# Kernel tuning notes

Measured on AMD Instinct MI355X. Metric: run time of the kernel, lower is better.

## Reference

```python
import jax, jax.numpy as jnp
import numpy as np

jax.config.update("jax_enable_x64", True)

# Module constants (from MySDELayer.call / run_model)
NUM_TRAJ = 512
DT = 2.0 ** (-8)          # deltat
NSTEPS = 255              # len(arange(0,1,DT)) - 1
OMEGA = 5.0265            # params[0]
GAMMA = 0.36              # params[2]
SQG = float(np.sqrt(GAMMA))


def setup_inputs() -> dict:
    key = jax.random.key(0)
    k1, k2 = jax.random.split(key)
    inputs = jax.random.normal(k1, (32, 1), dtype=jnp.float32)
    # unit-normal Wiener increments; scaled by sqrt(DT) inside reference
    wvec = jax.random.normal(k2, (32 * NUM_TRAJ, NSTEPS, 2), dtype=jnp.float32)
    return {"inputs": inputs, "wvec": wvec}


def _sde_probs(eps, dw):
    """Euler-Maruyama integration of the Genois qubit heterodyne SDE in Bloch
    coordinates (d=3 state, m=2 Wiener channels, complex128 as in the original),
    followed by unwrap to rho and Pauli-expectation probabilities.
    eps: [N] complex128 (per-trajectory middle parameter, e.g. detuning)
    dw:  [N, NSTEPS, 2] complex128 Wiener increments (stddev sqrt(DT))
    returns probs [N, NSTEPS+1, 6] float64
    """
    N = eps.shape[0]
    x0 = jnp.broadcast_to(jnp.array([0.0, 0.0, 1.0], dtype=jnp.complex128), (N, 3))

    def step(x, dwt):  # x: [N,3], dwt: [N,2]
        xx, yy, zz = x[:, 0], x[:, 1], x[:, 2]
        # drift: Rabi drive OMEGA about x, detuning eps about z, dephasing GAMMA
        drift = jnp.stack([
            -eps * yy - GAMMA * xx,
            eps * xx - OMEGA * zz - GAMMA * yy,
            OMEGA * yy,
        ], axis=1)
        # heterodyne measurement backaction (two quadratures)
        b1 = SQG * jnp.stack([-xx * zz, -yy * zz, 1.0 - zz * zz], axis=1)
        b2 = SQG * jnp.stack([-yy, xx, jnp.zeros_like(xx)], axis=1)
        xn = x + drift * DT + b1 * dwt[:, 0:1] + b2 * dwt[:, 1:2]
        return xn, xn

    _, xs = jax.lax.scan(step, x0, jnp.swapaxes(dw, 0, 1))  # [NSTEPS, N, 3]
    xvec = jnp.concatenate([x0[None], xs], axis=0)           # [T, N, 3]
    xvec = jnp.transpose(xvec, (1, 0, 2))                    # [N, T, 3]

    # unwrap_x_to_rho: rho = 0.5*(I + r.sigma) as length-4 vec
    rho = jnp.stack([
        0.5 * (1.0 + xvec[..., 2]),
        0.5 * (xvec[..., 0] - 1j * xvec[..., 1]),
        0.5 * (xvec[..., 0] + 1j * xvec[..., 1]),
        0.5 * (1.0 - xvec[..., 2]),
    ], axis=-1)                                              # [N, T, 4]

    # calc_exp with Pauli matrices
    ex = jnp.real(rho[..., 1] + rho[..., 2])
    ey = jnp.real(1j * (rho[..., 1] - rho[..., 2]))
    ez = jnp.real(rho[..., 0] - rho[..., 3])
    px, py, pz = 0.5 * (ex + 1.0), 0.5 * (ey + 1.0), 0.5 * (ez + 1.0)
    return jnp.stack([px, 1.0 - px, py, 1.0 - py, pz, 1.0 - pz], axis=2)  # [N,T,6]


def reference(inputs, wvec):
    B = inputs.shape[0]
    # tf.tile(inputs, [num_traj, 1])[:, 0] -> trajectory-major replication
    eps = jnp.tile(inputs, (NUM_TRAJ, 1))[:, 0].astype(jnp.complex128)  # [N]
    dw = (wvec * np.sqrt(DT)).astype(jnp.complex128)                    # [N,255,2]
    probs = _sde_probs(eps, dw)                                         # [N,T,6]
    probs_by_params = probs.reshape(B, NUM_TRAJ, probs.shape[1], 6)
    return jnp.mean(probs_by_params, axis=1)                            # [B,T,6]
```

## Files before the change

kernel.cpp:

```cpp
#include <hip/hip_runtime.h>

#define NSTEPS 255
#define TPTS   256
#define NTRAJ  16384
#define NBLK   256
#define CH     15

#define GAMMA_F 0.36f
#define OMEGA_F 5.0265f
#define DT_F    0.00390625f
#define CW      0.0375f
#define GD      (GAMMA_F * DT_F)
#define OD      (OMEGA_F * DT_F)

typedef __fp16 half2v __attribute__((ext_vector_type(2)));
typedef float  f32x2  __attribute__((ext_vector_type(2)));

__device__ __forceinline__ unsigned pk2(float a, float b) {
  half2v h = __builtin_amdgcn_cvt_pkrtz(a, b);
  return __builtin_bit_cast(unsigned, h);
}

template<int CTRL, int RM>
__device__ __forceinline__ float dpp_add(float v) {
  int sh = __builtin_amdgcn_update_dpp(0, __float_as_int(v), CTRL, RM, 0xf, true);
  return v + __int_as_float(sh);
}

__device__ __forceinline__ float wave_sum64(float v) {
  v = dpp_add<0x111, 0xf>(v);
  v = dpp_add<0x112, 0xf>(v);
  v = dpp_add<0x114, 0xf>(v);
  v = dpp_add<0x118, 0xf>(v);
  v = dpp_add<0x142, 0xa>(v);
  v = dpp_add<0x143, 0xc>(v);
  return v;
}

#define STEP(w2, tidx) {                                                        \
  const float w0  = (w2).x * CW;                                                \
  const f32x2 w1n = nCW2 * (w2).y;                        \
  const f32x2 sw  = __builtin_shufflevector(v, v, 1, 0);             \
  f32x2 t = __builtin_elementwise_fma(epack, sw, v);                            \
  t = __builtin_elementwise_fma(mGD2, v, t);                                    \
  const f32x2 p   = v * z;                                                      \
  const f32x2 mw0 = {-w0, -w0};                                                 \
  t = __builtin_elementwise_fma(p, mw0, t);                                     \
  t = __builtin_elementwise_fma(sw, w1n, t);                                    \
  t[1] = __builtin_fmaf(-OD, z, t[1]);                                          \
  const float a = __builtin_fmaf(OD, v[1], z);                                  \
  const float r = __builtin_fmaf(-(z * z), w0, w0);                             \
  v = t; z = a + r;                                                             \
  sp[(size_t)((tidx) - 1) * NTRAJ] = make_uint2(pk2(v[0], v[1]), pk2(z, 0.0f)); \
}

#define LOADC(BUF, CHUNK_) {                                                    \
  _Pragma("unroll")                                                             \
  for (int i_ = 0; i_ < CH; ++i_) BUF[i_] = wrow[(CHUNK_) * CH + i_];           \
}

#define PROC(BUF) {                                                             \
  _Pragma("unroll")                                                             \
  for (int i_ = 0; i_ < CH; ++i_) STEP(BUF[i_], tb + i_)                        \
  tb += CH;                                                                     \
}

__global__ __launch_bounds__(64) void sde_integrate(const float* __restrict__ inp,
                                                    const float* __restrict__ wvec,
                                                    uint2* __restrict__ buf) {
  const int g    = blockIdx.x;
  const int lane = threadIdx.x;
  const float eps = inp[lane & 31];
  const f32x2 epack = {-eps * DT_F, eps * DT_F};
  const f32x2 mGD2  = {-GD, -GD};
  const f32x2 nCW2  = {-CW, CW};

  const float2* __restrict__ wrow =
      reinterpret_cast<const float2*>(wvec) + (size_t)(g * 64 + lane) * NSTEPS;
  uint2* __restrict__ sp = buf + (size_t)(g * 64 + lane);

  f32x2 v = {0.0f, 0.0f};
  float z = 1.0f;

  float2 bufA[CH], bufB[CH], bufC[CH];

  LOADC(bufA, 0);
  LOADC(bufB, 1);
  int tb = 1;
  #pragma unroll 1
  for (int k = 0; k < 5; ++k) {
    LOADC(bufC, 3 * k + 2); PROC(bufA);
    LOADC(bufA, 3 * k + 3); PROC(bufB);
    LOADC(bufB, 3 * k + 4); PROC(bufC);
  }
  PROC(bufA);
  PROC(bufB);
}

__global__ __launch_bounds__(256) void sde_reduce(const uint2* __restrict__ buf,
                                                  float* __restrict__ out) {
  const int wid  = (blockIdx.x << 2) | (threadIdx.x >> 6);
  const int lane = threadIdx.x & 63;
  const int b = wid >> 8;
  const int t = wid & 255;
  float* o = out + (size_t)wid * 6;

  if (t == 0) {
    if (lane < 6) o[lane] = (lane == 4) ? 1.0f : ((lane == 5) ? 0.0f : 0.5f);
    return;
  }

  const uint2* base = buf + (size_t)(t - 1) * NTRAJ + (b << 9) + lane;
  float sx = 0.0f, sy = 0.0f, sz = 0.0f;
  #pragma unroll
  for (int k = 0; k < 8; ++k) {
    const uint2 w = base[(size_t)k * 64];
    const half2v xy = __builtin_bit_cast(half2v, w.x);
    const half2v zp = __builtin_bit_cast(half2v, w.y);
    sx += (float)xy[0];
    sy += (float)xy[1];
    sz += (float)zp[0];
  }
  sx = wave_sum64(sx);
  sy = wave_sum64(sy);
  sz = wave_sum64(sz);

  if (lane == 63) {
    const float inv = 1.0f / 512.0f;
    const float mx = sx * inv, my = sy * inv, mz = sz * inv;
    o[0] = 0.5f * (1.0f + mx);
    o[1] = 0.5f * (1.0f - mx);
    o[2] = 0.5f * (1.0f + my);
    o[3] = 0.5f * (1.0f - my);
    o[4] = 0.5f * (1.0f + mz);
    o[5] = 0.5f * (1.0f - mz);
  }
}

extern "C" void kernel_launch(void* const* d_in, const int* in_sizes, int n_in,
                              void* d_out, int out_size, void* d_ws, size_t ws_size,
                              hipStream_t stream) {
  (void)in_sizes; (void)n_in; (void)out_size; (void)ws_size;
  const float* inp  = (const float*)d_in[0];
  const float* wvec = (const float*)d_in[1];
  float* out  = (float*)d_out;
  uint2* buf  = (uint2*)d_ws;

  sde_integrate<<<NBLK, 64, 0, stream>>>(inp, wvec, buf);
  sde_reduce<<<2048, 256, 0, stream>>>(buf, out);
}
```

Measured before the change: 27.81 us.

## Stage Wiener increments through double-buffered LDS with coalesced global loads

Each trajectory used to read its own strided 2040-byte row of Wiener increments directly, so a wave's loads were uncoalesced. Now 16 lanes cooperatively load contiguous 8-byte pieces of each row into a padded, double-buffered LDS tile. Each thread then reads its own row back from LDS as float4 pairs, with the next chunk's global loads issued during the current chunk's compute. This adds LDS traffic and a per-chunk __syncthreads, and the fixed chunk offsets and bounds must cover exactly 255 steps.

```diff
diff --git a/kernel.cpp b/kernel.cpp
--- a/kernel.cpp
+++ b/kernel.cpp
@@ -4,7 +4,7 @@
 #define TPTS   256
 #define NTRAJ  16384
 #define NBLK   256
-#define CH     15
+#define ROWB   2040
 
 #define GAMMA_F 0.36f
 #define OMEGA_F 5.0265f
@@ -12,6 +12,9 @@
 #define CW      0.0375f
 #define GD      (GAMMA_F * DT_F)
 #define OD      (OMEGA_F * DT_F)
+
+#define LROW  144
+#define LBUF  (64 * LROW)
 
 typedef __fp16 half2v __attribute__((ext_vector_type(2)));
 typedef float  f32x2  __attribute__((ext_vector_type(2)));
@@ -37,9 +40,9 @@
   return v;
 }
 
-#define STEP(w2, tidx) {                                                        \
-  const float w0  = (w2).x * CW;                                                \
-  const f32x2 w1n = nCW2 * (w2).y;                        \
+#define STEP2(wx_, wy_) {                                                       \
+  const float w0  = (wx_) * CW;                                                 \
+  const f32x2 w1n = nCW2 * (wy_);                         \
   const f32x2 sw  = __builtin_shufflevector(v, v, 1, 0);             \
   f32x2 t = __builtin_elementwise_fma(epack, sw, v);                            \
   t = __builtin_elementwise_fma(mGD2, v, t);                                    \
@@ -48,53 +51,68 @@
   t = __builtin_elementwise_fma(p, mw0, t);                                     \
   t = __builtin_elementwise_fma(sw, w1n, t);                                    \
   t[1] = __builtin_fmaf(-OD, z, t[1]);                                          \
-  const float a = __builtin_fmaf(OD, v[1], z);                                  \
-  const float r = __builtin_fmaf(-(z * z), w0, w0);                             \
-  v = t; z = a + r;                                                             \
-  sp[(size_t)((tidx) - 1) * NTRAJ] = make_uint2(pk2(v[0], v[1]), pk2(z, 0.0f)); \
+  const float a_ = __builtin_fmaf(OD, v[1], z);                                 \
+  const float r_ = __builtin_fmaf(-(z * z), w0, w0);                            \
+  v = t; z = a_ + r_;                                                           \
+  *sp = make_uint2(pk2(v[0], v[1]), pk2(z, 0.0f));                              \
+  sp += NTRAJ;                                                                  \
 }
 
-#define LOADC(BUF, CHUNK_) {                                                    \
+#define GLOAD(co) {                                                             \
   _Pragma("unroll")                                                             \
-  for (int i_ = 0; i_ < CH; ++i_) BUF[i_] = wrow[(CHUNK_) * CH + i_];           \
+  for (int i_ = 0; i_ < 16; ++i_)                                               \
+    r2[i_] = *(const float2*)(wbp + (size_t)i_ * (4 * ROWB) + (co));            \
 }
 
-#define PROC(BUF) {                                                             \
+#define LDSWRITE() {                                                            \
   _Pragma("unroll")                                                             \
-  for (int i_ = 0; i_ < CH; ++i_) STEP(BUF[i_], tb + i_)                        \
-  tb += CH;                                                                     \
+  for (int i_ = 0; i_ < 16; ++i_)                                               \
+    *(float2*)(smem + wl + i_ * (4 * LROW)) = r2[i_];                           \
+}
+
+#define CHUNK(NK) {                                                             \
+  _Pragma("unroll")                                                             \
+  for (int p_ = 0; p_ < 8; ++p_) {                                              \
+    const float4 wv = *(const float4*)(smem + rl + p_ * 16);                    \
+    STEP2(wv.x, wv.y);                                                          \
+    if (2 * p_ + 1 < (NK)) STEP2(wv.z, wv.w);                                   \
+  }                                                                             \
 }
 
 __global__ __launch_bounds__(64) void sde_integrate(const float* __restrict__ inp,
                                                     const float* __restrict__ wvec,
                                                     uint2* __restrict__ buf) {
-  const int g    = blockIdx.x;
-  const int lane = threadIdx.x;
-  const float eps = inp[lane & 31];
+  __shared__ alignas(16) char smem[2 * LBUF];
+  const int g = blockIdx.x, l = threadIdx.x;
+  const float eps = inp[l & 31];
   const f32x2 epack = {-eps * DT_F, eps * DT_F};
   const f32x2 mGD2  = {-GD, -GD};
   const f32x2 nCW2  = {-CW, CW};
 
-  const float2* __restrict__ wrow =
-      reinterpret_cast<const float2*>(wvec) + (size_t)(g * 64 + lane) * NSTEPS;
-  uint2* __restrict__ sp = buf + (size_t)(g * 64 + lane);
+  const char* wbp = (const char*)wvec
+      + (size_t)(g * 64 + (l >> 4)) * ROWB + (l & 15) * 8;
+  unsigned wl = (unsigned)((l >> 4) * LROW + (l & 15) * 8);
+  unsigned rl = (unsigned)(l * LROW);
+  uint2* __restrict__ sp = buf + (g * 64 + l);
 
   f32x2 v = {0.0f, 0.0f};
   float z = 1.0f;
+  float2 r2[16];
 
-  float2 bufA[CH], bufB[CH], bufC[CH];
+  GLOAD(0);
+  LDSWRITE();
+  __syncthreads();
+  GLOAD(120);
+  CHUNK(15);
 
-  LOADC(bufA, 0);
-  LOADC(bufB, 1);
-  int tb = 1;
   #pragma unroll 1
-  for (int k = 0; k < 5; ++k) {
-    LOADC(bufC, 3 * k + 2); PROC(bufA);
-    LOADC(bufA, 3 * k + 3); PROC(bufB);
-    LOADC(bufB, 3 * k + 4); PROC(bufC);
+  for (int c = 1; c <= 15; ++c) {
+    wl ^= LBUF; rl ^= LBUF;
+    LDSWRITE();
+    __syncthreads();
+    if (c < 15) GLOAD(128 * c + 120);
+    CHUNK(16);
   }
-  PROC(bufA);
-  PROC(bufB);
 }
 
 __global__ __launch_bounds__(256) void sde_reduce(const uint2* __restrict__ buf,
```

Result: slower. 30.23 us (+8.7%).

## Stage trajectory states in LDS and pre-reduce per block before finalize

Applied to the files above, without the earlier changes.

Instead of writing every trajectory's packed state for every timestep to global workspace and reducing it in a second kernel, each 64-lane block now stores its states in shared memory and sums the 64 trajectories per timestep inside the block. The much smaller per-block partial sums are then combined across the 8 blocks of each batch by a small finalize kernel. This removes roughly 33MB of global write and read traffic. In exchange it uses about 132KB of LDS per block, which limits occupancy, and it adds a serial 64-element per-thread reduction tail after the integration loop.

```diff
diff --git a/kernel.cpp b/kernel.cpp
--- a/kernel.cpp
+++ b/kernel.cpp
@@ -13,6 +13,8 @@
 #define GD      (GAMMA_F * DT_F)
 #define OD      (OMEGA_F * DT_F)
 
+#define PITCH  520
+
 typedef __fp16 half2v __attribute__((ext_vector_type(2)));
 typedef float  f32x2  __attribute__((ext_vector_type(2)));
 
@@ -21,23 +23,7 @@
   return __builtin_bit_cast(unsigned, h);
 }
 
-template<int CTRL, int RM>
-__device__ __forceinline__ float dpp_add(float v) {
-  int sh = __builtin_amdgcn_update_dpp(0, __float_as_int(v), CTRL, RM, 0xf, true);
-  return v + __int_as_float(sh);
-}
-
-__device__ __forceinline__ float wave_sum64(float v) {
-  v = dpp_add<0x111, 0xf>(v);
-  v = dpp_add<0x112, 0xf>(v);
-  v = dpp_add<0x114, 0xf>(v);
-  v = dpp_add<0x118, 0xf>(v);
-  v = dpp_add<0x142, 0xa>(v);
-  v = dpp_add<0x143, 0xc>(v);
-  return v;
-}
-
-#define STEP(w2, tidx) {                                                        \
+#define STEP2(w2, ii_) {                                                        \
   const float w0  = (w2).x * CW;                                                \
   const f32x2 w1n = nCW2 * (w2).y;                        \
   const f32x2 sw  = __builtin_shufflevector(v, v, 1, 0);             \
@@ -48,10 +34,10 @@
   t = __builtin_elementwise_fma(p, mw0, t);                                     \
   t = __builtin_elementwise_fma(sw, w1n, t);                                    \
   t[1] = __builtin_fmaf(-OD, z, t[1]);                                          \
-  const float a = __builtin_fmaf(OD, v[1], z);                                  \
-  const float r = __builtin_fmaf(-(z * z), w0, w0);                             \
-  v = t; z = a + r;                                                             \
-  sp[(size_t)((tidx) - 1) * NTRAJ] = make_uint2(pk2(v[0], v[1]), pk2(z, 0.0f)); \
+  const float a_ = __builtin_fmaf(OD, v[1], z);                                 \
+  const float r_ = __builtin_fmaf(-(z * z), w0, w0);                            \
+  v = t; z = a_ + r_;                                                           \
+  *(uint2*)(sb + (ii_) * PITCH) = make_uint2(pk2(v[0], v[1]), pk2(z, 0.0f));    \
 }
 
 #define LOADC(BUF, CHUNK_) {                                                    \
@@ -61,23 +47,23 @@
 
 #define PROC(BUF) {                                                             \
   _Pragma("unroll")                                                             \
-  for (int i_ = 0; i_ < CH; ++i_) STEP(BUF[i_], tb + i_)                        \
-  tb += CH;                                                                     \
+  for (int i_ = 0; i_ < CH; ++i_) STEP2(BUF[i_], i_)                            \
+  sb += CH * PITCH;                                                             \
 }
 
 __global__ __launch_bounds__(64) void sde_integrate(const float* __restrict__ inp,
                                                     const float* __restrict__ wvec,
-                                                    uint2* __restrict__ buf) {
-  const int g    = blockIdx.x;
-  const int lane = threadIdx.x;
-  const float eps = inp[lane & 31];
+                                                    float* __restrict__ partial) {
+  __shared__ alignas(16) char smem[NSTEPS * PITCH];
+  const int g = blockIdx.x, l = threadIdx.x;
+  const float eps = inp[l & 31];
   const f32x2 epack = {-eps * DT_F, eps * DT_F};
   const f32x2 mGD2  = {-GD, -GD};
   const f32x2 nCW2  = {-CW, CW};
 
   const float2* __restrict__ wrow =
-      reinterpret_cast<const float2*>(wvec) + (size_t)(g * 64 + lane) * NSTEPS;
-  uint2* __restrict__ sp = buf + (size_t)(g * 64 + lane);
+      reinterpret_cast<const float2*>(wvec) + (size_t)(g * 64 + l) * NSTEPS;
+  char* sb = smem + l * 8;
 
   f32x2 v = {0.0f, 0.0f};
   float z = 1.0f;
@@ -86,7 +72,6 @@
 
   LOADC(bufA, 0);
   LOADC(bufB, 1);
-  int tb = 1;
   #pragma unroll 1
   for (int k = 0; k < 5; ++k) {
     LOADC(bufC, 3 * k + 2); PROC(bufA);
@@ -95,46 +80,57 @@
   }
   PROC(bufA);
   PROC(bufB);
+
+  __syncthreads();
+
+  #pragma unroll
+  for (int k = 0; k < 4; ++k) {
+    const int s = l + 64 * k;
+    if (s < NSTEPS) {
+      const char* rb = smem + (size_t)s * PITCH;
+      float fx = 0.0f, fy = 0.0f, fz = 0.0f;
+      #pragma unroll
+      for (int j = 0; j < 64; ++j) {
+        const uint2 u = *(const uint2*)(rb + j * 8);
+        const half2v xy = __builtin_bit_cast(half2v, u.x);
+        const half2v zp = __builtin_bit_cast(half2v, u.y);
+        fx += (float)xy[0];
+        fy += (float)xy[1];
+        fz += (float)zp[0];
+      }
+      float* p = partial + ((size_t)g * NSTEPS + s) * 3;
+      p[0] = fx; p[1] = fy; p[2] = fz;
+    }
+  }
 }
 
-__global__ __launch_bounds__(256) void sde_reduce(const uint2* __restrict__ buf,
-                                                  float* __restrict__ out) {
-  const int wid  = (blockIdx.x << 2) | (threadIdx.x >> 6);
-  const int lane = threadIdx.x & 63;
-  const int b = wid >> 8;
-  const int t = wid & 255;
-  float* o = out + (size_t)wid * 6;
+__global__ __launch_bounds__(256) void sde_finalize(const float* __restrict__ partial,
+                                                    float* __restrict__ out) {
+  const int idx = blockIdx.x * blockDim.x + threadIdx.x;
+  const int b = idx >> 8;
+  const int t = idx & 255;
+  float* o = out + (size_t)idx * 6;
 
   if (t == 0) {
-    if (lane < 6) o[lane] = (lane == 4) ? 1.0f : ((lane == 5) ? 0.0f : 0.5f);
+    o[0] = 0.5f; o[1] = 0.5f; o[2] = 0.5f; o[3] = 0.5f;
+    o[4] = 1.0f; o[5] = 0.0f;
     return;
   }
 
-  const uint2* base = buf + (size_t)(t - 1) * NTRAJ + (b << 9) + lane;
   float sx = 0.0f, sy = 0.0f, sz = 0.0f;
   #pragma unroll
-  for (int k = 0; k < 8; ++k) {
-    const uint2 w = base[(size_t)k * 64];
-    const half2v xy = __builtin_bit_cast(half2v, w.x);
-    const half2v zp = __builtin_bit_cast(half2v, w.y);
-    sx += (float)xy[0];
-    sy += (float)xy[1];
-    sz += (float)zp[0];
+  for (int j = 0; j < 8; ++j) {
+    const float* p = partial + ((size_t)(b * 8 + j) * NSTEPS + (t - 1)) * 3;
+    sx += p[0]; sy += p[1]; sz += p[2];
   }
-  sx = wave_sum64(sx);
-  sy = wave_sum64(sy);
-  sz = wave_sum64(sz);
-
-  if (lane == 63) {
-    const float inv = 1.0f / 512.0f;
-    const float mx = sx * inv, my = sy * inv, mz = sz * inv;
-    o[0] = 0.5f * (1.0f + mx);
-    o[1] = 0.5f * (1.0f - mx);
-    o[2] = 0.5f * (1.0f + my);
-    o[3] = 0.5f * (1.0f - my);
-    o[4] = 0.5f * (1.0f + mz);
-    o[5] = 0.5f * (1.0f - mz);
-  }
+  const float inv = 1.0f / 512.0f;
+  const float mx = sx * inv, my = sy * inv, mz = sz * inv;
+  o[0] = 0.5f * (1.0f + mx);
+  o[1] = 0.5f * (1.0f - mx);
+  o[2] = 0.5f * (1.0f + my);
+  o[3] = 0.5f * (1.0f - my);
+  o[4] = 0.5f * (1.0f + mz);
+  o[5] = 0.5f * (1.0f - mz);
 }
 
 extern "C" void kernel_launch(void* const* d_in, const int* in_sizes, int n_in,
@@ -143,9 +139,9 @@
   (void)in_sizes; (void)n_in; (void)out_size; (void)ws_size;
   const float* inp  = (const float*)d_in[0];
   const float* wvec = (const float*)d_in[1];
-  float* out  = (float*)d_out;
-  uint2* buf  = (uint2*)d_ws;
+  float* out     = (float*)d_out;
+  float* partial = (float*)d_ws;
 
-  sde_integrate<<<NBLK, 64, 0, stream>>>(inp, wvec, buf);
-  sde_reduce<<<2048, 256, 0, stream>>>(buf, out);
+  sde_integrate<<<NBLK, 64, 0, stream>>>(inp, wvec, partial);
+  sde_finalize<<<32, 256, 0, stream>>>(partial, out);
 }
```

Result: faster. 23.01 us (-17.3%).

## Fuse SDE integration and trajectory reduction into one kernel via LDS history

Applied to the files above, without the earlier changes.

Replaces the two-kernel design, which wrote a packed per-step state buffer to global memory and reduced it in a second kernel, with a single kernel. Each 512-thread block handles one batch element and all its trajectories. Each thread integrates 32 steps at a time into an LDS history window, and then all eight waves reduce that window and write the output. This removes the global round trip for the history and one launch. In exchange it runs only 32 blocks, adds block barriers inside the serial integration, and needs more registers for the 32-step double buffers.

```diff
diff --git a/kernel.cpp b/kernel.cpp
--- a/kernel.cpp
+++ b/kernel.cpp
@@ -1,10 +1,8 @@
 #include <hip/hip_runtime.h>
 
 #define NSTEPS 255
-#define TPTS   256
 #define NTRAJ  16384
-#define NBLK   256
-#define CH     15
+#define NGRP   32
 
 #define GAMMA_F 0.36f
 #define OMEGA_F 5.0265f
@@ -12,6 +10,9 @@
 #define CW      0.0375f
 #define GD      (GAMMA_F * DT_F)
 #define OD      (OMEGA_F * DT_F)
+
+#define HSLOT  4096
+#define HBYTES (32 * HSLOT)
 
 typedef __fp16 half2v __attribute__((ext_vector_type(2)));
 typedef float  f32x2  __attribute__((ext_vector_type(2)));
@@ -37,115 +38,121 @@
   return v;
 }
 
-#define STEP(w2, tidx) {                                                        \
-  const float w0  = (w2).x * CW;                                                \
-  const f32x2 w1n = nCW2 * (w2).y;                        \
+#define STEP2(wx_, wy_, ii_) {                                                  \
+  const float w0  = (wx_) * CW;                                                 \
+  const float cy  = (wy_) * CW;                                                 \
   const f32x2 sw  = __builtin_shufflevector(v, v, 1, 0);             \
   f32x2 t = __builtin_elementwise_fma(epack, sw, v);                            \
   t = __builtin_elementwise_fma(mGD2, v, t);                                    \
-  const f32x2 p   = v * z;                                                      \
-  const f32x2 mw0 = {-w0, -w0};                                                 \
-  t = __builtin_elementwise_fma(p, mw0, t);                                     \
-  t = __builtin_elementwise_fma(sw, w1n, t);                                    \
+  const f32x2 w0s = {w0, w0};                                                   \
+  t = __builtin_elementwise_fma(-(v * z), w0s, t);                              \
+  const f32x2 cys = {-cy, cy};                                                  \
+  t = __builtin_elementwise_fma(sw, cys, t);                                    \
   t[1] = __builtin_fmaf(-OD, z, t[1]);                                          \
-  const float a = __builtin_fmaf(OD, v[1], z);                                  \
-  const float r = __builtin_fmaf(-(z * z), w0, w0);                             \
-  v = t; z = a + r;                                                             \
-  sp[(size_t)((tidx) - 1) * NTRAJ] = make_uint2(pk2(v[0], v[1]), pk2(z, 0.0f)); \
+  const float a_ = __builtin_fmaf(OD, v[1], z);                                 \
+  const float r_ = __builtin_fmaf(-(z * z), w0, w0);                            \
+  v = t; z = a_ + r_;                                                           \
+  *(uint2*)(hb + (ii_) * HSLOT) = make_uint2(pk2(v[0], v[1]), pk2(z, 0.0f));    \
 }
 
-#define LOADC(BUF, CHUNK_) {                                                    \
+#define LOADW(BUF, WI, CNT) {                                                   \
   _Pragma("unroll")                                                             \
-  for (int i_ = 0; i_ < CH; ++i_) BUF[i_] = wrow[(CHUNK_) * CH + i_];           \
+  for (int i_ = 0; i_ < (CNT); ++i_) BUF[i_] = wrow[(WI) * 32 + i_];            \
 }
 
-#define PROC(BUF) {                                                             \
+#define PROCW(BUF, CNT) {                                                       \
   _Pragma("unroll")                                                             \
-  for (int i_ = 0; i_ < CH; ++i_) STEP(BUF[i_], tb + i_)                        \
-  tb += CH;                                                                     \
+  for (int i_ = 0; i_ < (CNT); ++i_) STEP2((BUF)[i_].x, (BUF)[i_].y, i_)        \
 }
 
-__global__ __launch_bounds__(64) void sde_integrate(const float* __restrict__ inp,
-                                                    const float* __restrict__ wvec,
-                                                    uint2* __restrict__ buf) {
-  const int g    = blockIdx.x;
-  const int lane = threadIdx.x;
-  const float eps = inp[lane & 31];
+#define TAILW(w_) {                                                             \
+  _Pragma("unroll")                                                             \
+  for (int k_ = 0; k_ < 4; ++k_) {                                              \
+    const int s_  = wid + 8 * k_;                                               \
+    const int st_ = (w_) * 32 + s_;                                             \
+    if (st_ < NSTEPS) {                                                         \
+      const char* rb_ = hist + s_ * HSLOT + l * 8;                              \
+      float fx_ = 0.0f, fy_ = 0.0f, fz_ = 0.0f;                                 \
+      _Pragma("unroll")                                                         \
+      for (int m_ = 0; m_ < 8; ++m_) {                                          \
+        const uint2 u_ = *(const uint2*)(rb_ + m_ * 512);                       \
+        const half2v xy_ = __builtin_bit_cast(half2v, u_.x);                    \
+        const half2v zp_ = __builtin_bit_cast(half2v, u_.y);                    \
+        fx_ += (float)xy_[0]; fy_ += (float)xy_[1]; fz_ += (float)zp_[0];       \
+      }                                                                         \
+      const float sx_ = wave_sum64(fx_);                                        \
+      const float sy_ = wave_sum64(fy_);                                        \
+      const float sz_ = wave_sum64(fz_);                                        \
+      if (l == 63) {                                                            \
+        const float inv_ = 1.0f / 512.0f;                                       \
+        const float mx_ = sx_ * inv_, my_ = sy_ * inv_, mz_ = sz_ * inv_;       \
+        float* o_ = out + ((size_t)b * 256 + st_ + 1) * 6;                      \
+        o_[0] = 0.5f * (1.0f + mx_); o_[1] = 0.5f * (1.0f - mx_);               \
+        o_[2] = 0.5f * (1.0f + my_); o_[3] = 0.5f * (1.0f - my_);               \
+        o_[4] = 0.5f * (1.0f + mz_); o_[5] = 0.5f * (1.0f - mz_);               \
+      }                                                                         \
+    }                                                                           \
+  }                                                                             \
+}
+
+__global__ __launch_bounds__(512, 2)
+void sde_all(const float* __restrict__ inp, const float* __restrict__ wvec,
+             float* __restrict__ out) {
+  __shared__ alignas(16) char hist[HBYTES];
+  const int b   = blockIdx.x;
+  const int tid = threadIdx.x;
+  const int wid = tid >> 6;
+  const int l   = tid & 63;
+
+  const float eps = inp[tid & 31];
   const f32x2 epack = {-eps * DT_F, eps * DT_F};
   const f32x2 mGD2  = {-GD, -GD};
-  const f32x2 nCW2  = {-CW, CW};
 
   const float2* __restrict__ wrow =
-      reinterpret_cast<const float2*>(wvec) + (size_t)(g * 64 + lane) * NSTEPS;
-  uint2* __restrict__ sp = buf + (size_t)(g * 64 + lane);
+      reinterpret_cast<const float2*>(wvec) + (size_t)(b * 512 + tid) * NSTEPS;
+  char* const hb = hist + tid * 8;
+
+  if (tid == 0) {
+    float* o = out + (size_t)b * 256 * 6;
+    o[0] = 0.5f; o[1] = 0.5f; o[2] = 0.5f; o[3] = 0.5f;
+    o[4] = 1.0f; o[5] = 0.0f;
+  }
 
   f32x2 v = {0.0f, 0.0f};
   float z = 1.0f;
+  float2 WA[32], WB[32];
 
-  float2 bufA[CH], bufB[CH], bufC[CH];
-
-  LOADC(bufA, 0);
-  LOADC(bufB, 1);
-  int tb = 1;
+  LOADW(WA, 0, 32);
   #pragma unroll 1
-  for (int k = 0; k < 5; ++k) {
-    LOADC(bufC, 3 * k + 2); PROC(bufA);
-    LOADC(bufA, 3 * k + 3); PROC(bufB);
-    LOADC(bufB, 3 * k + 4); PROC(bufC);
+  for (int k = 0; k < 3; ++k) {
+    LOADW(WB, 2 * k + 1, 32);
+    PROCW(WA, 32);
+    __syncthreads();
+    TAILW(2 * k);
+    __syncthreads();
+    LOADW(WA, 2 * k + 2, 32);
+    PROCW(WB, 32);
+    __syncthreads();
+    TAILW(2 * k + 1);
+    __syncthreads();
   }
-  PROC(bufA);
-  PROC(bufB);
-}
-
-__global__ __launch_bounds__(256) void sde_reduce(const uint2* __restrict__ buf,
-                                                  float* __restrict__ out) {
-  const int wid  = (blockIdx.x << 2) | (threadIdx.x >> 6);
-  const int lane = threadIdx.x & 63;
-  const int b = wid >> 8;
-  const int t = wid & 255;
-  float* o = out + (size_t)wid * 6;
-
-  if (t == 0) {
-    if (lane < 6) o[lane] = (lane == 4) ? 1.0f : ((lane == 5) ? 0.0f : 0.5f);
-    return;
-  }
-
-  const uint2* base = buf + (size_t)(t - 1) * NTRAJ + (b << 9) + lane;
-  float sx = 0.0f, sy = 0.0f, sz = 0.0f;
-  #pragma unroll
-  for (int k = 0; k < 8; ++k) {
-    const uint2 w = base[(size_t)k * 64];
-    const half2v xy = __builtin_bit_cast(half2v, w.x);
-    const half2v zp = __builtin_bit_cast(half2v, w.y);
-    sx += (float)xy[0];
-    sy += (float)xy[1];
-    sz += (float)zp[0];
-  }
-  sx = wave_sum64(sx);
-  sy = wave_sum64(sy);
-  sz = wave_sum64(sz);
-
-  if (lane == 63) {
-    const float inv = 1.0f / 512.0f;
-    const float mx = sx * inv, my = sy * inv, mz = sz * inv;
-    o[0] = 0.5f * (1.0f + mx);
-    o[1] = 0.5f * (1.0f - mx);
-    o[2] = 0.5f * (1.0f + my);
-    o[3] = 0.5f * (1.0f - my);
-    o[4] = 0.5f * (1.0f + mz);
-    o[5] = 0.5f * (1.0f - mz);
-  }
+  LOADW(WB, 7, 31);
+  PROCW(WA, 32);
+  __syncthreads();
+  TAILW(6);
+  __syncthreads();
+  PROCW(WB, 31);
+  __syncthreads();
+  TAILW(7);
 }
 
 extern "C" void kernel_launch(void* const* d_in, const int* in_sizes, int n_in,
                               void* d_out, int out_size, void* d_ws, size_t ws_size,
                               hipStream_t stream) {
-  (void)in_sizes; (void)n_in; (void)out_size; (void)ws_size;
+  (void)in_sizes; (void)n_in; (void)out_size; (void)d_ws; (void)ws_size;
   const float* inp  = (const float*)d_in[0];
   const float* wvec = (const float*)d_in[1];
-  float* out  = (float*)d_out;
-  uint2* buf  = (uint2*)d_ws;
+  float* out = (float*)d_out;
 
-  sde_integrate<<<NBLK, 64, 0, stream>>>(inp, wvec, buf);
-  sde_reduce<<<2048, 256, 0, stream>>>(buf, out);
+  sde_all<<<NGRP, 512, 0, stream>>>(inp, wvec, out);
 }
```

Measured after the change: 48.36 us. 73.9% more time.
